# Performance work log

Measured on AMD Instinct MI355X. Metric: run time of the kernel, lower is better.

Reference implementation:

```python
import jax, jax.numpy as jnp
import numpy as np

N = 500_000   # total nodes in batched graph
E = 10_000_000  # total edges
G = 1_000     # number of graphs in the batch
H = 8         # hidden_dim
C = 8         # n_classes


def setup_inputs() -> dict:
    key = jax.random.key(0)
    k1, k2, k3, k4, k5, k6 = jax.random.split(key, 6)
    src = jax.random.randint(k1, (E,), 0, N)
    dst = jax.random.randint(k2, (E,), 0, N)
    graph_ids = jnp.sort(jax.random.randint(k3, (N,), 0, G))
    W1 = jax.random.normal(k4, (1, H), dtype=jnp.float32) * 0.5
    W2 = jax.random.normal(k5, (H, H), dtype=jnp.float32) * 0.3
    Wlast = jax.random.normal(k6, (H, C), dtype=jnp.float32) * 0.3
    return {"W1": W1, "W2": W2, "Wlast": Wlast,
            "src": src, "dst": dst, "graph_ids": graph_ids}


def reference(W1, W2, Wlast, src, dst, graph_ids):
    ones_e = jnp.ones(src.shape[0], dtype=jnp.float32)
    deg_in = jax.ops.segment_sum(ones_e, dst, num_segments=N)   # in-degrees
    deg_out = jax.ops.segment_sum(ones_e, src, num_segments=N)  # out-degrees
    # DGL GraphConv norm='both': clamp degrees to >=1, then pow(-1/2)
    inv_sqrt_out = jnp.maximum(deg_out, 1.0) ** -0.5
    inv_sqrt_in = jnp.maximum(deg_in, 1.0) ** -0.5

    def gconv(h, W):
        # h: [N, d]; gather-scatter message passing, then dense transform
        h = h * inv_sqrt_out[:, None]
        agg = jax.ops.segment_sum(h[src], dst, num_segments=N)
        return (agg * inv_sqrt_in[:, None]) @ W

    h = deg_in[:, None]  # input feature = in_degrees, shape [N, 1]
    h = jax.nn.relu(gconv(h, W1))
    h = jax.nn.relu(gconv(h, W2))

    # dgl.mean_nodes: per-graph mean over nodes
    counts = jax.ops.segment_sum(jnp.ones(N, dtype=jnp.float32), graph_ids,
                                 num_segments=G)
    hg = jax.ops.segment_sum(h, graph_ids, num_segments=G)
    hg = hg / jnp.maximum(counts, 1.0)[:, None]
    return hg @ Wlast  # [G, n_classes], Linear with bias=False
```

## Files before the change

### kernel.cpp

```cpp
#include <hip/hip_runtime.h>


#define TB 256
#define STB 512
#define BSH 13
#define BNODES 8192
#define MAXNB 64
#define SCH 4096
#define SCH4 (SCH / 4)
#define EPT 8
#define CSTR 16
#define INVB 0xFFFFFFFFu

__global__ void init_kernel(unsigned* __restrict__ curD, unsigned* __restrict__ curS,
                            float* __restrict__ Xsum, int NB, unsigned CAP, int G) {
    int i = blockIdx.x * TB + threadIdx.x;
    if (i < NB) { curD[i * CSTR] = (unsigned)i * CAP; curS[i * CSTR] = (unsigned)i * CAP; }
    if (i < G) Xsum[i] = 0.0f;
}

__global__ void scatter_sort_kernel(const int* __restrict__ src, const int* __restrict__ dst,
                                    unsigned* __restrict__ curD, unsigned* __restrict__ curS,
                                    unsigned* __restrict__ dstP, unsigned short* __restrict__ srcP,
                                    int NB, int E) {
    __shared__ unsigned cntD[MAXNB], cntS[MAXNB];
    __shared__ unsigned deltaD[MAXNB], deltaS[MAXNB];
    __shared__ unsigned totD_s, totS_s;
    __shared__ unsigned payD[SCH];
    __shared__ unsigned short valS[SCH];
    __shared__ unsigned char mapD[SCH], mapS[SCH];

    int tid = threadIdx.x;
    if (tid < MAXNB) { cntD[tid] = 0u; cntS[tid] = 0u; }
    __syncthreads();

    unsigned sA[EPT], dA[EPT], bD[EPT], bS[EPT];
    int blk = blockIdx.x;
#pragma unroll
    for (int v = 0; v < 2; ++v) {
        int q = blk * SCH4 + v * STB + tid;
        int be = q * 4;
        if (be + 3 < E) {
            int4 s4 = ((const int4*)src)[q];
            int4 d4 = ((const int4*)dst)[q];
            sA[v*4+0] = (unsigned)s4.x; sA[v*4+1] = (unsigned)s4.y;
            sA[v*4+2] = (unsigned)s4.z; sA[v*4+3] = (unsigned)s4.w;
            dA[v*4+0] = (unsigned)d4.x; dA[v*4+1] = (unsigned)d4.y;
            dA[v*4+2] = (unsigned)d4.z; dA[v*4+3] = (unsigned)d4.w;
#pragma unroll
            for (int k = 0; k < 4; ++k) {
                bD[v*4+k] = dA[v*4+k] >> BSH;
                bS[v*4+k] = sA[v*4+k] >> BSH;
            }
        } else {
#pragma unroll
            for (int k = 0; k < 4; ++k) {
                int j = be + k;
                if (j < E) {
                    sA[v*4+k] = (unsigned)src[j];
                    dA[v*4+k] = (unsigned)dst[j];
                    bD[v*4+k] = dA[v*4+k] >> BSH;
                    bS[v*4+k] = sA[v*4+k] >> BSH;
                } else {
                    bD[v*4+k] = INVB; bS[v*4+k] = INVB;
                    sA[v*4+k] = 0u; dA[v*4+k] = 0u;
                }
            }
        }
    }

#pragma unroll
    for (int k = 0; k < EPT; ++k) {
        if (bD[k] != INVB) {
            atomicAdd(&cntD[bD[k]], 1u);
            atomicAdd(&cntS[bS[k]], 1u);
        }
    }
    __syncthreads();

    int wv = tid >> 6, ln = tid & 63;
    if (wv == 0) {
        unsigned x = (ln < NB) ? cntD[ln] : 0u;
        unsigned inc = x;
#pragma unroll
        for (int o = 1; o < 64; o <<= 1) {
            unsigned y = __shfl_up(inc, o, 64);
            if (ln >= o) inc += y;
        }
        unsigned exc = inc - x;
        if (ln < NB) {
            unsigned gb = atomicAdd(&curD[ln * CSTR], x);
            deltaD[ln] = gb - exc;
            cntD[ln] = exc;
        }
        if (ln == 63) totD_s = inc;
    } else if (wv == 1) {
        unsigned x = (ln < NB) ? cntS[ln] : 0u;
        unsigned inc = x;
#pragma unroll
        for (int o = 1; o < 64; o <<= 1) {
            unsigned y = __shfl_up(inc, o, 64);
            if (ln >= o) inc += y;
        }
        unsigned exc = inc - x;
        if (ln < NB) {
            unsigned gb = atomicAdd(&curS[ln * CSTR], x);
            deltaS[ln] = gb - exc;
            cntS[ln] = exc;
        }
        if (ln == 63) totS_s = inc;
    }
    __syncthreads();

#pragma unroll
    for (int k = 0; k < EPT; ++k) {
        if (bD[k] != INVB) {
            unsigned p = atomicAdd(&cntD[bD[k]], 1u);
            payD[p] = ((dA[k] & (BNODES - 1)) << 19) | sA[k];
            mapD[p] = (unsigned char)bD[k];
            unsigned p2 = atomicAdd(&cntS[bS[k]], 1u);
            valS[p2] = (unsigned short)(sA[k] & (BNODES - 1));
            mapS[p2] = (unsigned char)bS[k];
        }
    }
    __syncthreads();

    unsigned tD = totD_s, tS = totS_s;
    for (unsigned i = tid; i < tD; i += STB) {
        unsigned b = mapD[i];
        dstP[deltaD[b] + i] = payD[i];
    }
    for (unsigned i = tid; i < tS; i += STB) {
        unsigned b = mapS[i];
        srcP[deltaS[b] + i] = valS[i];
    }
}

__global__ void deghist_kernel(const unsigned short* __restrict__ srcP, const unsigned* __restrict__ dstP,
                               const unsigned* __restrict__ curS, const unsigned* __restrict__ curD,
                               unsigned CAP, unsigned* __restrict__ pDeg, int Jlg) {
    __shared__ unsigned h[BNODES];
    for (int t = threadIdx.x; t < BNODES; t += TB) h[t] = 0u;
    __syncthreads();
    int b = blockIdx.x >> Jlg;
    int j = blockIdx.x & ((1 << Jlg) - 1);
    unsigned s0 = (unsigned)b * CAP;
    unsigned cD = curD[b * CSTR] - s0;
    unsigned lo = (unsigned)(((unsigned long long)cD * (unsigned)j) >> Jlg);
    unsigned hi = (unsigned)(((unsigned long long)cD * (unsigned)(j + 1)) >> Jlg);
    for (unsigned i = lo + threadIdx.x; i < hi; i += TB)
        atomicAdd(&h[dstP[s0 + i] >> 19], 0x10000u);
    unsigned cS = curS[b * CSTR] - s0;
    lo = (unsigned)(((unsigned long long)cS * (unsigned)j) >> Jlg);
    hi = (unsigned)(((unsigned long long)cS * (unsigned)(j + 1)) >> Jlg);
    for (unsigned i = lo + threadIdx.x; i < hi; i += TB)
        atomicAdd(&h[srcP[s0 + i]], 1u);
    __syncthreads();
    unsigned* row = pDeg + (size_t)blockIdx.x * BNODES;
    for (int t = threadIdx.x; t < BNODES; t += TB) row[t] = h[t];
}

__global__ void prep_kernel(const unsigned* __restrict__ pDeg,
                            float* __restrict__ pio, float* __restrict__ h0s,
                            float* __restrict__ isiA, int Jlg, int Npad) {
    int i = blockIdx.x * TB + threadIdx.x;
    if (i >= Npad) return;
    int b = i >> BSH, l = i & (BNODES - 1);
    int J = 1 << Jlg;
    unsigned sum = 0;
    for (int j = 0; j < J; ++j)
        sum += pDeg[(size_t)((b << Jlg) + j) * BNODES + l];
    float din = (float)(sum >> 16), dout = (float)(sum & 0xFFFFu);
    float a  = 1.0f / sqrtf(fmaxf(din, 1.0f));
    float bo = 1.0f / sqrtf(fmaxf(dout, 1.0f));
    pio[i]  = a * bo;
    h0s[i]  = din * bo;
    isiA[i] = a;
}

__global__ void wh_kernel(const unsigned* __restrict__ dstP, const unsigned* __restrict__ curD,
                          unsigned CAP, const float* __restrict__ table,
                          float* __restrict__ pOut, int Jlg) {
    __shared__ float h[BNODES];
    for (int t = threadIdx.x; t < BNODES; t += TB) h[t] = 0.0f;
    __syncthreads();
    int b = blockIdx.x >> Jlg;
    int j = blockIdx.x & ((1 << Jlg) - 1);
    unsigned s0 = (unsigned)b * CAP;
    unsigned cD = curD[b * CSTR] - s0;
    unsigned lo = (unsigned)(((unsigned long long)cD * (unsigned)j) >> Jlg);
    unsigned hi = (unsigned)(((unsigned long long)cD * (unsigned)(j + 1)) >> Jlg);
    for (unsigned i = lo + threadIdx.x; i < hi; i += TB) {
        unsigned e = dstP[s0 + i];
        atomicAdd(&h[e >> 19], table[e & 0x7FFFFu]);
    }
    __syncthreads();
    float* row = pOut + (size_t)blockIdx.x * BNODES;
    for (int t = threadIdx.x; t < BNODES; t += TB) row[t] = h[t];
}

__global__ void mid_kernel(const float* __restrict__ pC, const float* __restrict__ pio,
                           float* __restrict__ sarr, int Jlg, int Npad) {
    int i = blockIdx.x * TB + threadIdx.x;
    if (i >= Npad) return;
    int b = i >> BSH, l = i & (BNODES - 1);
    int J = 1 << Jlg;
    float t1 = 0.0f;
    for (int j = 0; j < J; ++j)
        t1 += pC[(size_t)((b << Jlg) + j) * BNODES + l];
    sarr[i] = t1 * pio[i];
}

__global__ void poolfinal_kernel(const float* __restrict__ pT, const float* __restrict__ isiA,
                                 const int* __restrict__ graph_ids,
                                 float* __restrict__ Xsum, int Jlg, int N) {
    int i = blockIdx.x * TB + threadIdx.x;
    bool valid = i < N;
    int ii = valid ? i : (N - 1);
    int b = ii >> BSH, l = ii & (BNODES - 1);
    int J = 1 << Jlg;
    float t2 = 0.0f;
    for (int j = 0; j < J; ++j)
        t2 += pT[(size_t)((b << Jlg) + j) * BNODES + l];
    float x = valid ? t2 * isiA[ii] : 0.0f;
    int g = graph_ids[ii];
    int g0 = __shfl(g, 0, 64);
    bool uniform = __all((!valid) || (g == g0));
    if (uniform) {
#pragma unroll
        for (int off = 32; off >= 1; off >>= 1) x += __shfl_down(x, off, 64);
        if ((threadIdx.x & 63) == 0) atomicAdd(&Xsum[g0], x);
    } else if (valid) {
        atomicAdd(&Xsum[g], x);
    }
}

__global__ void final_kernel(const float* __restrict__ Xsum, const int* __restrict__ graph_ids,
                             const float* __restrict__ W1, const float* __restrict__ W2,
                             const float* __restrict__ Wlast,
                             float* __restrict__ out, int N, int GC) {
    int i = blockIdx.x * TB + threadIdx.x;
    if (i < GC) {
        int g = i >> 3, j = i & 7;
        int lo = 0, hi = N;
        while (lo < hi) { int m = (lo + hi) >> 1; if (graph_ids[m] < g) lo = m + 1; else hi = m; }
        int lo2 = lo, hi2 = N;
        while (lo2 < hi2) { int m = (lo2 + hi2) >> 1; if (graph_ids[m] < g + 1) lo2 = m + 1; else hi2 = m; }
        float c = (float)(lo2 - lo);
        float r = 0.0f;
#pragma unroll
        for (int cc = 0; cc < 8; ++cc) {
            float m = 0.0f;
#pragma unroll
            for (int k = 0; k < 8; ++k) m += fmaxf(W1[k], 0.0f) * W2[k * 8 + cc];
            r += fmaxf(m, 0.0f) * Wlast[cc * 8 + j];
        }
        out[i] = Xsum[g] / fmaxf(c, 1.0f) * r;
    }
}


__global__ void fb_deg_kernel(const int* __restrict__ src, const int* __restrict__ dst,
                              float* __restrict__ deg_out, float* __restrict__ deg_in, int E) {
    int i = blockIdx.x * TB + threadIdx.x;
    if (i < E) {
        atomicAdd(&deg_out[src[i]], 1.0f);
        atomicAdd(&deg_in[dst[i]], 1.0f);
    }
}

__global__ void fb_prep_kernel(const float* __restrict__ deg_in, const float* __restrict__ deg_out,
                               float* __restrict__ isi, float* __restrict__ iso,
                               float* __restrict__ h0s, int N) {
    int i = blockIdx.x * TB + threadIdx.x;
    if (i < N) {
        float di = deg_in[i], dn = deg_out[i];
        float a = 1.0f / sqrtf(fmaxf(di, 1.0f));
        float b = 1.0f / sqrtf(fmaxf(dn, 1.0f));
        isi[i] = a; iso[i] = b; h0s[i] = di * b;
    }
}

__global__ void fb_conv_kernel(const int* __restrict__ src, const int* __restrict__ dst,
                               const float* __restrict__ vals, float* __restrict__ t, int E) {
    int i = blockIdx.x * TB + threadIdx.x;
    if (i < E) atomicAdd(&t[dst[i]], vals[src[i]]);
}

__global__ void fb_mid_kernel(const float* __restrict__ agg1, const float* __restrict__ isi,
                              const float* __restrict__ iso, float* __restrict__ s, int N) {
    int i = blockIdx.x * TB + threadIdx.x;
    if (i < N) s[i] = agg1[i] * isi[i] * iso[i];
}

__global__ void fb_pool_kernel(const float* __restrict__ t2, const float* __restrict__ isi,
                               const int* __restrict__ graph_ids,
                               float* __restrict__ Xsum, float* __restrict__ counts, int N) {
    int i = blockIdx.x * TB + threadIdx.x;
    bool valid = i < N;
    int ii = valid ? i : (N - 1);
    float x = valid ? t2[ii] * isi[ii] : 0.0f;
    float cnt = valid ? 1.0f : 0.0f;
    int g = graph_ids[ii];
    int g0 = __shfl(g, 0, 64);
    bool uniform = __all((!valid) || (g == g0));
    if (uniform) {
#pragma unroll
        for (int off = 32; off >= 1; off >>= 1) {
            x += __shfl_down(x, off, 64);
            cnt += __shfl_down(cnt, off, 64);
        }
        if ((threadIdx.x & 63) == 0) { atomicAdd(&Xsum[g0], x); atomicAdd(&counts[g0], cnt); }
    } else if (valid) {
        atomicAdd(&Xsum[g], x); atomicAdd(&counts[g], 1.0f);
    }
}

__global__ void fb_final_kernel(const float* __restrict__ Xsum, const float* __restrict__ counts,
                                const float* __restrict__ W1, const float* __restrict__ W2,
                                const float* __restrict__ Wlast, float* __restrict__ out, int GC) {
    int i = blockIdx.x * TB + threadIdx.x;
    if (i < GC) {
        int g = i >> 3, j = i & 7;
        float r = 0.0f;
#pragma unroll
        for (int c = 0; c < 8; ++c) {
            float m = 0.0f;
#pragma unroll
            for (int k = 0; k < 8; ++k) m += fmaxf(W1[k], 0.0f) * W2[k * 8 + c];
            r += fmaxf(m, 0.0f) * Wlast[c * 8 + j];
        }
        out[i] = Xsum[g] / fmaxf(counts[g], 1.0f) * r;
    }
}


extern "C" void kernel_launch(void* const* d_in, const int* in_sizes, int n_in,
                              void* d_out, int out_size, void* d_ws, size_t ws_size,
                              hipStream_t stream) {
    const float* W1        = (const float*)d_in[0];
    const float* W2        = (const float*)d_in[1];
    const float* Wlast     = (const float*)d_in[2];
    const int*   src       = (const int*)d_in[3];
    const int*   dst       = (const int*)d_in[4];
    const int*   graph_ids = (const int*)d_in[5];
    float* out = (float*)d_out;

    const int E = in_sizes[3];
    const int N = in_sizes[5];
    const int G = out_size / 8;

    int NB   = (N + BNODES - 1) >> BSH;
    int Npad = NB << BSH;
    int NCH  = (E + SCH - 1) / SCH;
    unsigned CAP = (unsigned)(((E / (NB > 0 ? NB : 1)) + 8192 + 511) & ~511);

    int Jlg = 3;
    size_t req = 0;
    size_t o_dstP, o_srcP, o_curD, o_curS, o_part, o_pio, o_h0sar, o_isi, o_Xsum;
    for (;; --Jlg) {
        int J = 1 << Jlg;
        size_t off = 0;
        auto A = [&](size_t bytes) { size_t o = off; off = (off + bytes + 127) & ~(size_t)127; return o; };
        o_dstP  = A((size_t)NB * CAP * 4);
        o_srcP  = A((size_t)NB * CAP * 2);
        o_curD  = A((size_t)NB * CSTR * 4);
        o_curS  = A((size_t)NB * CSTR * 4);
        o_part  = A((size_t)NB * J * BNODES * 4);
        o_pio   = A((size_t)Npad * 4);
        o_h0sar = A((size_t)Npad * 4);
        o_isi   = A((size_t)Npad * 4);
        o_Xsum  = A((size_t)G * 4);
        req = off;
        if (req <= ws_size || Jlg == 0) break;
    }

    bool fast = (N <= (1 << 19)) && (NB <= MAXNB) && (ws_size >= req) && (E >= 1);

    char* bp = (char*)d_ws;

    if (fast) {
        unsigned*       dstP = (unsigned*)(bp + o_dstP);
        unsigned short* srcP = (unsigned short*)(bp + o_srcP);
        unsigned* curD = (unsigned*)(bp + o_curD);
        unsigned* curS = (unsigned*)(bp + o_curS);
        unsigned* pDeg = (unsigned*)(bp + o_part);
        float*    pC   = (float*)(bp + o_part);
        float*    pT   = (float*)(bp + o_part);
        float* pio  = (float*)(bp + o_pio);
        float* h0s  = (float*)(bp + o_h0sar);
        float* sarr = (float*)(bp + o_h0sar);
        float* isiA = (float*)(bp + o_isi);
        float* Xsum = (float*)(bp + o_Xsum);

        int gridNp = (Npad + TB - 1) / TB;
        int gridN  = (N + TB - 1) / TB;
        int J = 1 << Jlg;
        int gridI = (max(NB, G) + TB - 1) / TB;

        init_kernel<<<gridI, TB, 0, stream>>>(curD, curS, Xsum, NB, CAP, G);
        scatter_sort_kernel<<<NCH, STB, 0, stream>>>(src, dst, curD, curS, dstP, srcP, NB, E);
        deghist_kernel<<<NB * J, TB, 0, stream>>>(srcP, dstP, curS, curD, CAP, pDeg, Jlg);
        prep_kernel<<<gridNp, TB, 0, stream>>>(pDeg, pio, h0s, isiA, Jlg, Npad);
        wh_kernel<<<NB * J, TB, 0, stream>>>(dstP, curD, CAP, h0s, pC, Jlg);
        mid_kernel<<<gridNp, TB, 0, stream>>>(pC, pio, sarr, Jlg, Npad);
        wh_kernel<<<NB * J, TB, 0, stream>>>(dstP, curD, CAP, sarr, pT, Jlg);
        poolfinal_kernel<<<gridN, TB, 0, stream>>>(pT, isiA, graph_ids, Xsum, Jlg, N);
        final_kernel<<<(out_size + TB - 1) / TB, TB, 0, stream>>>(Xsum, graph_ids,
                                                                  W1, W2, Wlast, out, N, out_size);
    } else {
        float* ws = (float*)d_ws;
        size_t f = 0;
        auto FA = [&](size_t n) { size_t o = f; f += (n + 3) & ~(size_t)3; return o; };
        size_t f_degin  = FA(N);
        size_t f_degout = FA(N);
        size_t f_agg1   = FA(N);
        size_t f_t2     = FA(N);
        size_t f_Xsum   = FA(G);
        size_t f_cnt    = FA(G);
        size_t zf = f;
        size_t f_isi = FA(N);
        size_t f_iso = FA(N);
        size_t f_h0s = FA(N);
        size_t f_s   = FA(N);
        hipMemsetAsync(ws, 0, zf * sizeof(float), stream);
        int gridE = (E + TB - 1) / TB;
        int gridN = (N + TB - 1) / TB;
        int gridO = (out_size + TB - 1) / TB;
        fb_deg_kernel<<<gridE, TB, 0, stream>>>(src, dst, ws + f_degout, ws + f_degin, E);
        fb_prep_kernel<<<gridN, TB, 0, stream>>>(ws + f_degin, ws + f_degout,
                                                 ws + f_isi, ws + f_iso, ws + f_h0s, N);
        fb_conv_kernel<<<gridE, TB, 0, stream>>>(src, dst, ws + f_h0s, ws + f_agg1, E);
        fb_mid_kernel<<<gridN, TB, 0, stream>>>(ws + f_agg1, ws + f_isi, ws + f_iso, ws + f_s, N);
        fb_conv_kernel<<<gridE, TB, 0, stream>>>(src, dst, ws + f_s, ws + f_t2, E);
        fb_pool_kernel<<<gridN, TB, 0, stream>>>(ws + f_t2, ws + f_isi, graph_ids,
                                                 ws + f_Xsum, ws + f_cnt, N);
        fb_final_kernel<<<gridO, TB, 0, stream>>>(ws + f_Xsum, ws + f_cnt, W1, W2, Wlast,
                                                  out, out_size);
    }
}
```

Before: 391.5 us.

## Use nontemporal loads, bigger histogram blocks, more partitions, split scatter launch

Several loads of streamed data (edge inputs, sorted srcP, partial histograms, and dstP on its last use) now use nontemporal hints so they pollute the cache less. The histogram and weighted-histogram kernels switch to 512-thread blocks, and the partition count per bucket rises from 8 to 16 to add parallelism. The scatter-sort launch is split into two half-grid launches. The extra partitions add partial-sum traffic and workspace use in the reduce kernels, and the second launch adds launch overhead.

```diff
diff --git a/kernel.cpp b/kernel.cpp
--- a/kernel.cpp
+++ b/kernel.cpp
@@ -2,6 +2,7 @@
 
 
 #define TB 256
+#define DTB 512
 #define STB 512
 #define BSH 13
 #define BNODES 8192
@@ -12,6 +13,8 @@
 #define CSTR 16
 #define INVB 0xFFFFFFFFu
 
+typedef __attribute__((ext_vector_type(4))) int int4v;
+
 __global__ void init_kernel(unsigned* __restrict__ curD, unsigned* __restrict__ curS,
                             float* __restrict__ Xsum, int NB, unsigned CAP, int G) {
     int i = blockIdx.x * TB + threadIdx.x;
@@ -22,7 +25,7 @@
 __global__ void scatter_sort_kernel(const int* __restrict__ src, const int* __restrict__ dst,
                                     unsigned* __restrict__ curD, unsigned* __restrict__ curS,
                                     unsigned* __restrict__ dstP, unsigned short* __restrict__ srcP,
-                                    int NB, int E) {
+                                    int NB, int E, int blk0) {
     __shared__ unsigned cntD[MAXNB], cntS[MAXNB];
     __shared__ unsigned deltaD[MAXNB], deltaS[MAXNB];
     __shared__ unsigned totD_s, totS_s;
@@ -35,20 +38,18 @@
     __syncthreads();
 
     unsigned sA[EPT], dA[EPT], bD[EPT], bS[EPT];
-    int blk = blockIdx.x;
+    int blk = blockIdx.x + blk0;
 #pragma unroll
     for (int v = 0; v < 2; ++v) {
         int q = blk * SCH4 + v * STB + tid;
         int be = q * 4;
         if (be + 3 < E) {
-            int4 s4 = ((const int4*)src)[q];
-            int4 d4 = ((const int4*)dst)[q];
-            sA[v*4+0] = (unsigned)s4.x; sA[v*4+1] = (unsigned)s4.y;
-            sA[v*4+2] = (unsigned)s4.z; sA[v*4+3] = (unsigned)s4.w;
-            dA[v*4+0] = (unsigned)d4.x; dA[v*4+1] = (unsigned)d4.y;
-            dA[v*4+2] = (unsigned)d4.z; dA[v*4+3] = (unsigned)d4.w;
+            int4v s4 = __builtin_nontemporal_load((const int4v*)src + q);
+            int4v d4 = __builtin_nontemporal_load((const int4v*)dst + q);
 #pragma unroll
             for (int k = 0; k < 4; ++k) {
+                sA[v*4+k] = (unsigned)s4[k];
+                dA[v*4+k] = (unsigned)d4[k];
                 bD[v*4+k] = dA[v*4+k] >> BSH;
                 bS[v*4+k] = sA[v*4+k] >> BSH;
             }
@@ -140,7 +141,7 @@
                                const unsigned* __restrict__ curS, const unsigned* __restrict__ curD,
                                unsigned CAP, unsigned* __restrict__ pDeg, int Jlg) {
     __shared__ unsigned h[BNODES];
-    for (int t = threadIdx.x; t < BNODES; t += TB) h[t] = 0u;
+    for (int t = threadIdx.x; t < BNODES; t += DTB) h[t] = 0u;
     __syncthreads();
     int b = blockIdx.x >> Jlg;
     int j = blockIdx.x & ((1 << Jlg) - 1);
@@ -148,16 +149,16 @@
     unsigned cD = curD[b * CSTR] - s0;
     unsigned lo = (unsigned)(((unsigned long long)cD * (unsigned)j) >> Jlg);
     unsigned hi = (unsigned)(((unsigned long long)cD * (unsigned)(j + 1)) >> Jlg);
-    for (unsigned i = lo + threadIdx.x; i < hi; i += TB)
+    for (unsigned i = lo + threadIdx.x; i < hi; i += DTB)
         atomicAdd(&h[dstP[s0 + i] >> 19], 0x10000u);
     unsigned cS = curS[b * CSTR] - s0;
     lo = (unsigned)(((unsigned long long)cS * (unsigned)j) >> Jlg);
     hi = (unsigned)(((unsigned long long)cS * (unsigned)(j + 1)) >> Jlg);
-    for (unsigned i = lo + threadIdx.x; i < hi; i += TB)
-        atomicAdd(&h[srcP[s0 + i]], 1u);
+    for (unsigned i = lo + threadIdx.x; i < hi; i += DTB)
+        atomicAdd(&h[__builtin_nontemporal_load(&srcP[s0 + i])], 1u);
     __syncthreads();
     unsigned* row = pDeg + (size_t)blockIdx.x * BNODES;
-    for (int t = threadIdx.x; t < BNODES; t += TB) row[t] = h[t];
+    for (int t = threadIdx.x; t < BNODES; t += DTB) row[t] = h[t];
 }
 
 __global__ void prep_kernel(const unsigned* __restrict__ pDeg,
@@ -169,7 +170,7 @@
     int J = 1 << Jlg;
     unsigned sum = 0;
     for (int j = 0; j < J; ++j)
-        sum += pDeg[(size_t)((b << Jlg) + j) * BNODES + l];
+        sum += __builtin_nontemporal_load(&pDeg[(size_t)((b << Jlg) + j) * BNODES + l]);
     float din = (float)(sum >> 16), dout = (float)(sum & 0xFFFFu);
     float a  = 1.0f / sqrtf(fmaxf(din, 1.0f));
     float bo = 1.0f / sqrtf(fmaxf(dout, 1.0f));
@@ -178,11 +179,12 @@
     isiA[i] = a;
 }
 
+template <int LAST>
 __global__ void wh_kernel(const unsigned* __restrict__ dstP, const unsigned* __restrict__ curD,
                           unsigned CAP, const float* __restrict__ table,
                           float* __restrict__ pOut, int Jlg) {
     __shared__ float h[BNODES];
-    for (int t = threadIdx.x; t < BNODES; t += TB) h[t] = 0.0f;
+    for (int t = threadIdx.x; t < BNODES; t += DTB) h[t] = 0.0f;
     __syncthreads();
     int b = blockIdx.x >> Jlg;
     int j = blockIdx.x & ((1 << Jlg) - 1);
@@ -190,13 +192,13 @@
     unsigned cD = curD[b * CSTR] - s0;
     unsigned lo = (unsigned)(((unsigned long long)cD * (unsigned)j) >> Jlg);
     unsigned hi = (unsigned)(((unsigned long long)cD * (unsigned)(j + 1)) >> Jlg);
-    for (unsigned i = lo + threadIdx.x; i < hi; i += TB) {
-        unsigned e = dstP[s0 + i];
+    for (unsigned i = lo + threadIdx.x; i < hi; i += DTB) {
+        unsigned e = LAST ? __builtin_nontemporal_load(&dstP[s0 + i]) : dstP[s0 + i];
         atomicAdd(&h[e >> 19], table[e & 0x7FFFFu]);
     }
     __syncthreads();
     float* row = pOut + (size_t)blockIdx.x * BNODES;
-    for (int t = threadIdx.x; t < BNODES; t += TB) row[t] = h[t];
+    for (int t = threadIdx.x; t < BNODES; t += DTB) row[t] = h[t];
 }
 
 __global__ void mid_kernel(const float* __restrict__ pC, const float* __restrict__ pio,
@@ -207,7 +209,7 @@
     int J = 1 << Jlg;
     float t1 = 0.0f;
     for (int j = 0; j < J; ++j)
-        t1 += pC[(size_t)((b << Jlg) + j) * BNODES + l];
+        t1 += __builtin_nontemporal_load(&pC[(size_t)((b << Jlg) + j) * BNODES + l]);
     sarr[i] = t1 * pio[i];
 }
 
@@ -221,7 +223,7 @@
     int J = 1 << Jlg;
     float t2 = 0.0f;
     for (int j = 0; j < J; ++j)
-        t2 += pT[(size_t)((b << Jlg) + j) * BNODES + l];
+        t2 += __builtin_nontemporal_load(&pT[(size_t)((b << Jlg) + j) * BNODES + l]);
     float x = valid ? t2 * isiA[ii] : 0.0f;
     int g = graph_ids[ii];
     int g0 = __shfl(g, 0, 64);
@@ -355,7 +357,7 @@
     int NCH  = (E + SCH - 1) / SCH;
     unsigned CAP = (unsigned)(((E / (NB > 0 ? NB : 1)) + 8192 + 511) & ~511);
 
-    int Jlg = 3;
+    int Jlg = 4;
     size_t req = 0;
     size_t o_dstP, o_srcP, o_curD, o_curS, o_part, o_pio, o_h0sar, o_isi, o_Xsum;
     for (;; --Jlg) {
@@ -398,13 +400,18 @@
         int J = 1 << Jlg;
         int gridI = (max(NB, G) + TB - 1) / TB;
 
+        int NCH1 = (NCH + 1) / 2;
+        int NCH2 = NCH - NCH1;
+
         init_kernel<<<gridI, TB, 0, stream>>>(curD, curS, Xsum, NB, CAP, G);
-        scatter_sort_kernel<<<NCH, STB, 0, stream>>>(src, dst, curD, curS, dstP, srcP, NB, E);
-        deghist_kernel<<<NB * J, TB, 0, stream>>>(srcP, dstP, curS, curD, CAP, pDeg, Jlg);
+        scatter_sort_kernel<<<NCH1, STB, 0, stream>>>(src, dst, curD, curS, dstP, srcP, NB, E, 0);
+        if (NCH2 > 0)
+            scatter_sort_kernel<<<NCH2, STB, 0, stream>>>(src, dst, curD, curS, dstP, srcP, NB, E, NCH1);
+        deghist_kernel<<<NB * J, DTB, 0, stream>>>(srcP, dstP, curS, curD, CAP, pDeg, Jlg);
         prep_kernel<<<gridNp, TB, 0, stream>>>(pDeg, pio, h0s, isiA, Jlg, Npad);
-        wh_kernel<<<NB * J, TB, 0, stream>>>(dstP, curD, CAP, h0s, pC, Jlg);
+        wh_kernel<0><<<NB * J, DTB, 0, stream>>>(dstP, curD, CAP, h0s, pC, Jlg);
         mid_kernel<<<gridNp, TB, 0, stream>>>(pC, pio, sarr, Jlg, Npad);
-        wh_kernel<<<NB * J, TB, 0, stream>>>(dstP, curD, CAP, sarr, pT, Jlg);
+        wh_kernel<1><<<NB * J, DTB, 0, stream>>>(dstP, curD, CAP, sarr, pT, Jlg);
         poolfinal_kernel<<<gridN, TB, 0, stream>>>(pT, isiA, graph_ids, Xsum, Jlg, N);
         final_kernel<<<(out_size + TB - 1) / TB, TB, 0, stream>>>(Xsum, graph_ids,
                                                                   W1, W2, Wlast, out, N, out_size);
```

Result: faster. 379.6 us (-3.1%).
